# Kernel tuning notes

Hardware: AMD Instinct MI355X
Metric: run time of the kernel (lower is better)

Reference implementation:

```python
import jax, jax.numpy as jnp
import numpy as np

LEADER_IDX = 0
SOCIAL_DIST = 1.5
COHESION = 0.8
B, N, T = 64, 64, 100


def setup_inputs() -> dict:
    key = jax.random.key(0)
    k1, k2, k3, k4, k5 = jax.random.split(key, 5)
    # trajectories: (x, y, vel, yaw, acc, yawvel)
    x = jax.random.normal(k1, (B, N, T, 6), dtype=jnp.float32) * 5.0
    # world_from_agent: per-agent SE(2) homogeneous transform (B, 3, 3)
    theta = jax.random.uniform(k2, (B,), minval=-np.pi, maxval=np.pi)
    c, s = jnp.cos(theta), jnp.sin(theta)
    trans = jax.random.normal(k3, (B, 2), dtype=jnp.float32) * 50.0
    wfa = (jnp.zeros((B, 3, 3), dtype=jnp.float32)
           .at[:, 0, 0].set(c).at[:, 0, 1].set(-s)
           .at[:, 1, 0].set(s).at[:, 1, 1].set(c)
           .at[:, :2, 2].set(trans).at[:, 2, 2].set(1.0))
    # externalized randomness of torch forward (randint over B-1 choices, rand<p)
    rand_idx = jax.random.randint(k4, (T * N, B), 0, B - 1, dtype=jnp.int32)
    drop_mask = jax.random.uniform(k5, (T * N, B)) < COHESION
    return {"x": x, "world_from_agent": wfa, "rand_idx": rand_idx, "drop_mask": drop_mask}


def reference(x, world_from_agent, rand_idx, drop_mask):
    pos = x[..., :2]                                   # (B, N, T, 2)
    R = world_from_agent[:, :2, :2]                    # (B, 2, 2)
    t = world_from_agent[:, :2, 2]                     # (B, 2)
    pos_g = jnp.einsum('bntj,bij->bnti', pos, R) + t[:, None, None, :]
    # leader positions are detached (no grad), but same value in fwd
    leader = (jnp.arange(B) == LEADER_IDX)[:, None, None, None]
    pos_g = jnp.where(leader, jax.lax.stop_gradient(pos_g), pos_g)
    # (B,N,T,2) -> (T,N,B,2) -> (T*N, B, 2)  (matches torch transpose(0,2).reshape)
    flat = jnp.transpose(pos_g, (2, 1, 0, 3)).reshape(T * N, B, 2)
    # pairwise euclidean distances via norm trick (avoids (TN,B,B,2) diff tensor)
    sq = jnp.sum(flat * flat, axis=-1)                 # (TN, B)
    d2 = sq[:, :, None] + sq[:, None, :] - 2.0 * jnp.einsum('tbd,tcd->tbc', flat, flat)
    dist = jnp.sqrt(jnp.maximum(d2, 1e-12))            # (TN, B, B)
    eye = jnp.eye(B, dtype=bool)
    dist = jnp.where(eye[None], jnp.inf, dist)         # mask self-distance
    min_nb = jnp.argmin(dist, axis=-1).astype(jnp.int32)      # (TN, B)
    # row b of neighbor_choices is [0..b-1, b+1..B-1]; gather at rand_idx ->
    # value = rand_idx + (rand_idx >= b)
    b_idx = jnp.arange(B, dtype=jnp.int32)[None, :]
    rand_nb = rand_idx + (rand_idx >= b_idx).astype(jnp.int32)
    nb = jnp.where(drop_mask, rand_nb, min_nb)         # (TN, B)
    nd = jnp.take_along_axis(dist, nb[..., None], axis=2)[..., 0]  # (TN, B)
    nd = jnp.transpose(nd.reshape(T, N, B), (2, 1, 0))  # (B, N, T)
    loss = jnp.mean((nd - SOCIAL_DIST) ** 2, axis=-1)   # (B, N)
    return loss
```

## Files before the change

kernel.cpp:

```cpp
#include <hip/hip_runtime.h>

#define BB 64
#define NN 64
#define TT 100
#define WV 16
#define SP (BB + 1)

__global__ __launch_bounds__(1024) void social_fused_kernel(
    const float* __restrict__ x,
    const float* __restrict__ wfa,
    const int* __restrict__ rand_idx,
    const int* __restrict__ drop_mask,
    float* __restrict__ out)
{
    const int n   = blockIdx.x;
    const int tid = threadIdx.x;

    __shared__ float2 S[TT * SP];
    __shared__ float  Rld[WV][BB];

    {
        const int lb = tid >> 4;
        const int k  = tid & 15;
        const float* wp = wfa + lb * 9;
        const float r00 = wp[0], r01 = wp[1], tx = wp[2];
        const float r10 = wp[3], r11 = wp[4], ty = wp[5];
        const size_t xb = (((size_t)lb * NN + n) * (size_t)TT) * 6;
        #pragma unroll
        for (int j = 0; j < 7; ++j) {
            const int t = k + 16 * j;
            if (t < TT) {
                const float2 p = *(const float2*)(x + xb + (size_t)t * 6);
                const float gx = r00 * p.x + r01 * p.y + tx;
                const float gy = r10 * p.x + r11 * p.y + ty;
                S[t * SP + lb] = make_float2(gx, gy);
            }
        }
    }
    __syncthreads();

    const int w = tid >> 6;
    const int b = tid & 63;
    const float INF = __int_as_float(0x7f800000);

    float acc = 0.f;
    for (int t = w; t < TT; t += WV) {
        const int s = t * NN + n;
        const size_t sb = (size_t)s * BB + b;
        const int r  = rand_idx[sb];
        const int dm = drop_mask[sb];

        const float2* St = S + t * SP;
        const float2 g = St[b];
        const float gx = g.x, gy = g.y;

        float m0 = INF, m1 = INF, m2 = INF, m3 = INF;
        #pragma unroll
        for (int i = 0; i < 16; ++i) {
            {
                const int c = i;
                const float2 q = St[c];
                const float dx = gx - q.x, dy = gy - q.y;
                float d2 = fmaf(dx, dx, dy * dy);
                d2 = (c == b) ? INF : d2;
                m0 = fminf(m0, d2);
            }
            {
                const int c = 16 + i;
                const float2 q = St[c];
                const float dx = gx - q.x, dy = gy - q.y;
                float d2 = fmaf(dx, dx, dy * dy);
                d2 = (c == b) ? INF : d2;
                m1 = fminf(m1, d2);
            }
            {
                const int c = 32 + i;
                const float2 q = St[c];
                const float dx = gx - q.x, dy = gy - q.y;
                float d2 = fmaf(dx, dx, dy * dy);
                d2 = (c == b) ? INF : d2;
                m2 = fminf(m2, d2);
            }
            {
                const int c = 48 + i;
                const float2 q = St[c];
                const float dx = gx - q.x, dy = gy - q.y;
                float d2 = fmaf(dx, dx, dy * dy);
                d2 = (c == b) ? INF : d2;
                m3 = fminf(m3, d2);
            }
        }
        const float best = fminf(fminf(m0, m1), fminf(m2, m3));

        const int rnb = r + (r >= b ? 1 : 0);
        const float sq  = fmaf(gx, gx, gy * gy);
        const float qx  = __shfl(gx, rnb);
        const float qy  = __shfl(gy, rnb);
        const float qsq = __shfl(sq, rnb);
        const float d2r = fmaf(-2.0f, fmaf(gx, qx, gy * qy), sq + qsq);

        const float d2sel = dm ? d2r : best;
        const float nd = sqrtf(fmaxf(d2sel, 1e-12f));
        const float diff = nd - 1.5f;
        acc += diff * diff;
    }
    Rld[w][b] = acc;
    __syncthreads();

    if (w == 0) {
        float ssum = 0.f;
        #pragma unroll
        for (int jj = 0; jj < WV; ++jj)
            ssum += Rld[jj][b];
        out[(size_t)b * NN + n] = ssum * (1.0f / TT);
    }
}

extern "C" void kernel_launch(void* const* d_in, const int* in_sizes, int n_in,
                              void* d_out, int out_size, void* d_ws, size_t ws_size,
                              hipStream_t stream) {
    const float* x = (const float*)d_in[0];
    const float* wfa = (const float*)d_in[1];
    const int* rand_idx = (const int*)d_in[2];
    const int* drop_mask = (const int*)d_in[3];
    float* out = (float*)d_out;
    (void)d_ws; (void)ws_size;

    social_fused_kernel<<<NN, 1024, 0, stream>>>(x, wfa, rand_idx, drop_mask, out);
}
```

Measured before the change: 81.65 us.

## Split agent dimension across four blocks per n to raise grid parallelism

The launch grows from 64 blocks to 256. Each block now handles 16 of the 64 agents for one n, and each wave covers 4 timesteps times 16 agents. The goal is to fill more of the GPU's compute units, since 64 blocks cannot occupy the whole device. In exchange, every block still loads and transforms all 64 agents' positions into shared memory, so the global loads of x and the transform work are repeated four times. The random neighbor is now read from shared memory instead of taken by a wave shuffle, and partial sums are reduced with shuffles before a smaller shared-memory reduction.

```diff
diff --git a/kernel.cpp b/kernel.cpp
--- a/kernel.cpp
+++ b/kernel.cpp
@@ -13,11 +13,12 @@
     const int* __restrict__ drop_mask,
     float* __restrict__ out)
 {
-    const int n   = blockIdx.x;
+    const int n   = blockIdx.x & 63;
+    const int bq  = blockIdx.x >> 6;
     const int tid = threadIdx.x;
 
     __shared__ float2 S[TT * SP];
-    __shared__ float  Rld[WV][BB];
+    __shared__ float  Rw[WV][16];
 
     {
         const int lb = tid >> 4;
@@ -39,80 +40,89 @@
     }
     __syncthreads();
 
-    const int w = tid >> 6;
-    const int b = tid & 63;
+    const int w  = tid >> 6;
+    const int ln = tid & 63;
+    const int tq = ln >> 4;
+    const int bl = ln & 15;
+    const int b  = bq * 16 + bl;
+
     const float INF = __int_as_float(0x7f800000);
+    float acc = 0.f;
 
-    float acc = 0.f;
-    for (int t = w; t < TT; t += WV) {
-        const int s = t * NN + n;
-        const size_t sb = (size_t)s * BB + b;
-        const int r  = rand_idx[sb];
-        const int dm = drop_mask[sb];
+    #pragma unroll
+    for (int it = 0; it < 2; ++it) {
+        const int t = it * 64 + w * 4 + tq;
+        if (t < TT) {
+            const size_t sb = (size_t)(t * NN + n) * BB + b;
+            const int r  = rand_idx[sb];
+            const int dm = drop_mask[sb];
 
-        const float2* St = S + t * SP;
-        const float2 g = St[b];
-        const float gx = g.x, gy = g.y;
+            const float2* St = S + t * SP;
+            const float2 g = St[b];
+            const float gx = g.x, gy = g.y;
 
-        float m0 = INF, m1 = INF, m2 = INF, m3 = INF;
-        #pragma unroll
-        for (int i = 0; i < 16; ++i) {
-            {
-                const int c = i;
-                const float2 q = St[c];
-                const float dx = gx - q.x, dy = gy - q.y;
-                float d2 = fmaf(dx, dx, dy * dy);
-                d2 = (c == b) ? INF : d2;
-                m0 = fminf(m0, d2);
+            float m0 = INF, m1 = INF, m2 = INF, m3 = INF;
+            #pragma unroll
+            for (int i = 0; i < 16; ++i) {
+                {
+                    const int c = i;
+                    const float2 q = St[c];
+                    const float dx = gx - q.x, dy = gy - q.y;
+                    float d2 = fmaf(dx, dx, dy * dy);
+                    d2 = (c == b) ? INF : d2;
+                    m0 = fminf(m0, d2);
+                }
+                {
+                    const int c = 16 + i;
+                    const float2 q = St[c];
+                    const float dx = gx - q.x, dy = gy - q.y;
+                    float d2 = fmaf(dx, dx, dy * dy);
+                    d2 = (c == b) ? INF : d2;
+                    m1 = fminf(m1, d2);
+                }
+                {
+                    const int c = 32 + i;
+                    const float2 q = St[c];
+                    const float dx = gx - q.x, dy = gy - q.y;
+                    float d2 = fmaf(dx, dx, dy * dy);
+                    d2 = (c == b) ? INF : d2;
+                    m2 = fminf(m2, d2);
+                }
+                {
+                    const int c = 48 + i;
+                    const float2 q = St[c];
+                    const float dx = gx - q.x, dy = gy - q.y;
+                    float d2 = fmaf(dx, dx, dy * dy);
+                    d2 = (c == b) ? INF : d2;
+                    m3 = fminf(m3, d2);
+                }
             }
-            {
-                const int c = 16 + i;
-                const float2 q = St[c];
-                const float dx = gx - q.x, dy = gy - q.y;
-                float d2 = fmaf(dx, dx, dy * dy);
-                d2 = (c == b) ? INF : d2;
-                m1 = fminf(m1, d2);
-            }
-            {
-                const int c = 32 + i;
-                const float2 q = St[c];
-                const float dx = gx - q.x, dy = gy - q.y;
-                float d2 = fmaf(dx, dx, dy * dy);
-                d2 = (c == b) ? INF : d2;
-                m2 = fminf(m2, d2);
-            }
-            {
-                const int c = 48 + i;
-                const float2 q = St[c];
-                const float dx = gx - q.x, dy = gy - q.y;
-                float d2 = fmaf(dx, dx, dy * dy);
-                d2 = (c == b) ? INF : d2;
-                m3 = fminf(m3, d2);
-            }
+            const float best = fminf(fminf(m0, m1), fminf(m2, m3));
+
+            const int rnb = r + (r >= b ? 1 : 0);
+            const float sq  = fmaf(gx, gx, gy * gy);
+            const float2 qn = St[rnb];
+            const float qsq = fmaf(qn.x, qn.x, qn.y * qn.y);
+            const float d2r = fmaf(-2.0f, fmaf(gx, qn.x, gy * qn.y), sq + qsq);
+
+            const float d2sel = dm ? d2r : best;
+            const float nd = sqrtf(fmaxf(d2sel, 1e-12f));
+            const float diff = nd - 1.5f;
+            acc += diff * diff;
         }
-        const float best = fminf(fminf(m0, m1), fminf(m2, m3));
+    }
 
-        const int rnb = r + (r >= b ? 1 : 0);
-        const float sq  = fmaf(gx, gx, gy * gy);
-        const float qx  = __shfl(gx, rnb);
-        const float qy  = __shfl(gy, rnb);
-        const float qsq = __shfl(sq, rnb);
-        const float d2r = fmaf(-2.0f, fmaf(gx, qx, gy * qy), sq + qsq);
-
-        const float d2sel = dm ? d2r : best;
-        const float nd = sqrtf(fmaxf(d2sel, 1e-12f));
-        const float diff = nd - 1.5f;
-        acc += diff * diff;
-    }
-    Rld[w][b] = acc;
+    acc += __shfl_down(acc, 32);
+    acc += __shfl_down(acc, 16);
+    if (ln < 16) Rw[w][ln] = acc;
     __syncthreads();
 
-    if (w == 0) {
+    if (tid < 16) {
         float ssum = 0.f;
         #pragma unroll
         for (int jj = 0; jj < WV; ++jj)
-            ssum += Rld[jj][b];
-        out[(size_t)b * NN + n] = ssum * (1.0f / TT);
+            ssum += Rw[jj][tid];
+        out[(size_t)(bq * 16 + tid) * NN + n] = ssum * (1.0f / TT);
     }
 }
 
@@ -126,5 +136,6 @@
     float* out = (float*)d_out;
     (void)d_ws; (void)ws_size;
 
-    social_fused_kernel<<<NN, 1024, 0, stream>>>(x, wfa, rand_idx, drop_mask, out);
+    social_fused_kernel<<<NN * 4, 1024, 0, stream>>>(
+        x, wfa, rand_idx, drop_mask, out);
 }
```

After: 69.79 us. 14.5% less time.
